# Kernel tuning notes

Measured on AMD Instinct MI355X. Metric: run time of the kernel, lower is better.

## Reference

```python
import jax, jax.numpy as jnp
import numpy as np

N_NODES = 1024
N_FEAT = 12        # must equal LOOKBACK (U1 @ B @ U2.T constraint in original code)
LOOKBACK = 12
N_DATA = 8
KSIZE = 2
DILATIONS = [1, 3, 3, 3]
DELTA_MIN = 0.05
TIME_FEATS = 36    # 15 + 5 + 4 + 12


def setup_inputs() -> dict:
    key = jax.random.key(0)
    ks = jax.random.split(key, 21)
    f32 = jnp.float32

    def rn(k, shape, fan_in):
        return jax.random.normal(k, shape, dtype=f32) / np.sqrt(fan_in)

    return {
        'observation': jax.random.normal(ks[0], (N_NODES, N_DATA, LOOKBACK), dtype=f32),
        'time_features': jax.random.normal(ks[1], (TIME_FEATS,), dtype=f32),
        # main FC stack: (n_nodes*n_data) -> fc1 -> fc2 -> n_nodes*n_feat
        'fc_w1': rn(ks[2], (N_NODES * N_DATA, 2048), N_NODES * N_DATA),
        'fc_b1': jnp.zeros((2048,), f32),
        'fc_w2': rn(ks[3], (2048, 2048), 2048),
        'fc_b2': jnp.zeros((2048,), f32),
        'fc_w3': rn(ks[4], (2048, N_NODES * N_FEAT), 2048),
        'fc_b3': jnp.zeros((N_NODES * N_FEAT,), f32),
        # graph conv weights
        'W_forward': rn(ks[5], (KSIZE, N_FEAT, N_FEAT), N_FEAT),
        'W_backward': rn(ks[6], (KSIZE, N_FEAT, N_FEAT), N_FEAT),
        'b': jnp.zeros((N_FEAT,), f32),
        # GraphConstructor params (one fixed set, reused for every adjacency)
        'layer_initial': rn(ks[7], (LOOKBACK, N_NODES), N_NODES),
        'gs_w1': rn(ks[8], (N_NODES, 256), N_NODES),
        'gs_b1': jnp.zeros((256,), f32),
        'gs_w2': rn(ks[9], (256, N_NODES * N_FEAT), 256),
        'gs_b2': jnp.zeros((N_NODES * N_FEAT,), f32),
        'gt_w1': rn(ks[10], (TIME_FEATS, 256), TIME_FEATS),
        'gt_b1': jnp.zeros((256,), f32),
        'gt_w2': rn(ks[11], (256, N_NODES * N_FEAT), 256),
        'gt_b2': jnp.zeros((N_NODES * N_FEAT,), f32),
        'B': jax.random.normal(ks[12], (N_FEAT, N_FEAT), dtype=f32) / N_FEAT,
    }


def _forward(observation, time_features, fc_w1, fc_b1, fc_w2, fc_b2, fc_w3, fc_b3,
             W_forward, W_backward, b, layer_initial,
             gs_w1, gs_b1, gs_w2, gs_b2, gt_w1, gt_b1, gt_w2, gt_b2, B):
    relu = jax.nn.relu

    # fully_connected: observation (N, D, L) -> X (N, F, L)
    obs = jnp.transpose(observation, (2, 0, 1)).reshape(LOOKBACK, -1)  # (L, N*D)
    h = relu(obs @ fc_w1 + fc_b1)
    h = relu(h @ fc_w2 + fc_b2)
    h = relu(h @ fc_w3 + fc_b3)                                        # (L, N*F)
    X0 = jnp.transpose(h.reshape(LOOKBACK, N_NODES, N_FEAT), (1, 2, 0))  # (N, F, L)

    # node embedding U (N, L, F), computed once (graph params fixed)
    sp = relu(relu(layer_initial @ gs_w1 + gs_b1) @ gs_w2 + gs_b2)     # (L, N*F)
    tp = relu(relu(time_features @ gt_w1 + gt_b1) @ gt_w2 + gt_b2)     # (N*F,)
    U = jnp.transpose((sp + tp).reshape(LOOKBACK, N_NODES, N_FEAT), (1, 0, 2))

    adj_cache = {}

    def norm_adj(a, c):
        # normalized adjacency between feature-slices a and c (static ints)
        if (a, c) in adj_cache:
            return adj_cache[(a, c)]
        U1 = U[:, :, a]                      # (N, L)
        U2 = U[:, :, c]                      # (N, L)
        x = U1 @ B @ U2.T                    # (N, N); valid since L == F
        x = jnp.where(x >= DELTA_MIN, x, 0.0)
        A = jax.nn.softmax(x, axis=1)        # torch F.softmax default dim=1 for 2D
        # degree = diag(rowsum); inv(sqrtm(diag)) = diag(1/sqrt(rowsum))
        d = 1.0 / jnp.sqrt(A.sum(-1))
        out = A * d[:, None] * d[None, :]
        adj_cache[(a, c)] = out
        return out

    def conv(X, t):
        Z = jnp.zeros((N_NODES, N_FEAT), jnp.float32)
        for k in range(KSIZE):
            X_t = X[:, :, t - k]             # (N, F)
            L1 = norm_adj(t - k, t)
            L2 = norm_adj(t + k, t)
            x = L1 @ X_t @ W_forward[k] + L2 @ X_t @ W_backward[k] + b
            Z = Z + jax.nn.relu(x)
        return Z

    def conv_layer(X, d):
        cols = []
        for t in range(1, LOOKBACK - 1):
            if t % d == 0:
                cols.append(conv(X, t))
            else:
                cols.append(jnp.zeros((N_NODES, N_FEAT), jnp.float32))
        return jnp.stack(cols, axis=-1)      # (N, F, L-2)

    Z0 = conv_layer(X0, DILATIONS[0])
    Z1 = conv_layer(Z0, DILATIONS[1])
    Z2 = conv_layer(Z1, DILATIONS[2])
    Z3 = conv_layer(Z2, DILATIONS[3])
    return (Z0[:, :, -1], Z1[:, :, -1], Z2[:, :, -1], Z3[:, :, -1])


def reference(observation, time_features, fc_w1, fc_b1, fc_w2, fc_b2, fc_w3, fc_b3,
              W_forward, W_backward, b, layer_initial,
              gs_w1, gs_b1, gs_w2, gs_b2, gt_w1, gt_b1, gt_w2, gt_b2, B):
    return _forward(observation, time_features, fc_w1, fc_b1, fc_w2, fc_b2, fc_w3, fc_b3,
                    W_forward, W_backward, b, layer_initial,
                    gs_w1, gs_b1, gs_w2, gs_b2, gt_w1, gt_b1, gt_w2, gt_b2, B)
```

## Files before the change

kernel.cpp:

```cpp
#include <hip/hip_runtime.h>

#define OFF_SPP   0
#define OFF_TPH   49152
#define OFF_P1    65536
#define OFF_P2    327680
#define OFF_X     458752
#define OFF_UP    524288
#define OFF_TPP   1703936
#define OFF_U     1802240

template<int KS, int PIN, int P, int GATHER, int ATOM>
__device__ __forceinline__ void gemm_body(
    const float* __restrict__ xin, const float* __restrict__ bias_in,
    const float* __restrict__ W, float* __restrict__ part,
    int N, int K, int bx, int by, float* lx, float* red)
{
  int tid = threadIdx.x;
  int k0 = by * KS;
  for (int i = tid; i < 2*KS; i += 256) {
    int t = i / KS, kk = i - t*KS;
    float v;
    if (GATHER) {
      int k = k0 + kk;
      v = xin[(k >> 3)*96 + (k & 7)*12 + 9 + t];
    } else if (PIN == 0) {
      v = xin[t*K + k0 + kk];
    } else {
      v = 0.f;
      const float* p0 = xin + (size_t)(t*K + k0 + kk)*PIN;
      #pragma unroll
      for (int pp = 0; pp < PIN; ++pp) v += p0[pp];
    }
    if (bias_in) { v += bias_in[k0 + kk]; v = v > 0.f ? v : 0.f; }
    lx[i] = v;
  }
  __syncthreads();
  int kg = tid >> 5, cg2 = tid & 31;
  int colbase = bx*128 + cg2*4;
  float a0=0,a1=0,a2=0,a3=0,c0=0,c1=0,c2=0,c3=0;
  const int ksub = KS/8;
  for (int kk = kg*ksub; kk < kg*ksub + ksub; ++kk) {
    float4 w = *(const float4*)(W + (size_t)(k0+kk)*N + colbase);
    float x0 = lx[kk], x1 = lx[KS + kk];
    a0=fmaf(x0,w.x,a0); a1=fmaf(x0,w.y,a1); a2=fmaf(x0,w.z,a2); a3=fmaf(x0,w.w,a3);
    c0=fmaf(x1,w.x,c0); c1=fmaf(x1,w.y,c1); c2=fmaf(x1,w.z,c2); c3=fmaf(x1,w.w,c3);
  }
  float* rp = red + (kg*32 + cg2)*8;
  rp[0]=a0; rp[1]=a1; rp[2]=a2; rp[3]=a3; rp[4]=c0; rp[5]=c1; rp[6]=c2; rp[7]=c3;
  __syncthreads();
  int cg3 = tid & 31, q = tid >> 5;
  float s = 0.f;
  #pragma unroll
  for (int g = 0; g < 8; ++g) s += red[(g*32 + cg3)*8 + q];
  int t = q >> 2, c = q & 3;
  if (ATOM) {
    atomicAdd(part + (size_t)t*N + bx*128 + cg3*4 + c, s);
  } else {
    part[(size_t)(t*N + bx*128 + cg3*4 + c)*P + by] = s;
  }
}

__global__ void __launch_bounds__(256) k_front(
    const float* __restrict__ obs, const float* __restrict__ fc_w1,
    float* __restrict__ part1,
    const float* __restrict__ li, const float* __restrict__ gs_w1,
    const float* __restrict__ tf, const float* __restrict__ gt_w1,
    const float* __restrict__ gt_b1, const float* __restrict__ fc_b3,
    float* __restrict__ sp_part, float* __restrict__ tp_h,
    float* __restrict__ X_raw, float* __restrict__ out_tail)
{
  __shared__ float smem[2304];
  int b = blockIdx.x, tid = threadIdx.x;
  if (b < 1024) {
    gemm_body<128, 0, 64, 1, 0>(obs, (const float*)nullptr, fc_w1, part1,
                                2048, 8192, b & 15, b >> 4, smem, smem + 256);
  } else if (b < 1040) {
    float (*lil)[128] = (float(*)[128])smem;
    int sb = b - 1024;
    int cb = sb & 1, kc = sb >> 1;
    for (int i = tid; i < 1536; i += 256) {
      int r = i >> 7, kk = i & 127;
      lil[r][kk] = li[r*1024 + kc*128 + kk];
    }
    __syncthreads();
    int col = cb*128 + (tid & 127);
    int kh = tid >> 7;
    float acc[12];
    #pragma unroll
    for (int t=0;t<12;++t) acc[t]=0.f;
    for (int kk = kh*64; kk < kh*64 + 64; ++kk) {
      float w = gs_w1[(size_t)(kc*128 + kk)*256 + col];
      #pragma unroll
      for (int t=0;t<12;++t) acc[t] = fmaf(lil[t][kk], w, acc[t]);
    }
    int c = kc*2 + kh;
    #pragma unroll
    for (int t=0;t<12;++t) sp_part[(c*12 + t)*256 + col] = acc[t];
    for (int i = tid; i < 2304; i += 256) out_tail[sb*2304 + i] = 0.f;
    for (int i = tid; i < 1536; i += 256) {
      int idx = sb*1536 + i;
      int colx = idx >= 12288 ? idx - 12288 : idx;
      X_raw[idx] = fc_b3[colx];
    }
  } else {
    float acc = 0.f;
    for (int k = 0; k < 36; ++k)
      acc = fmaf(tf[k], gt_w1[k*256 + tid], acc);
    float v = acc + gt_b1[tid];
    tp_h[tid] = v > 0.f ? v : 0.f;
  }
}

__global__ void __launch_bounds__(256) k_umid(
    const float* __restrict__ part1, const float* __restrict__ fc_b1,
    const float* __restrict__ fc_w2, float* __restrict__ part2,
    const float* __restrict__ sp_part, const float* __restrict__ gs_b1,
    const float* __restrict__ tp_h,
    const float* __restrict__ gs_w2, const float* __restrict__ gt_w2,
    float* __restrict__ U_part, float* __restrict__ tp_part)
{
  __shared__ float smem[2176];
  int b = blockIdx.x, tid = threadIdx.x;
  if (b < 512) {
    gemm_body<64, 64, 32, 0, 0>(part1, fc_b1, fc_w2, part2, 2048, 2048,
                                b & 15, b >> 4, smem, smem + 128);
    return;
  }
  float* spl = smem;
  float* tpl = smem + 96;
  int ug = b - 512;
  int n  = (ug & 3)*256 + tid;
  int uy = ug >> 2;
  int k0 = uy*8;
  if (tid < 96) {
    int kk = tid / 12, t = tid % 12;
    float v = gs_b1[k0 + kk];
    #pragma unroll
    for (int c = 0; c < 16; ++c) v += sp_part[(c*12 + t)*256 + k0 + kk];
    spl[kk*12 + t] = v > 0.f ? v : 0.f;
  }
  if (tid < 8) tpl[tid] = tp_h[k0 + tid];
  __syncthreads();
  float sA[3][12];
  float tA[3] = {0.f, 0.f, 0.f};
  #pragma unroll
  for (int ap=0;ap<3;++ap)
    #pragma unroll
    for (int t=0;t<12;++t) sA[ap][t]=0.f;
  #pragma unroll
  for (int kk = 0; kk < 8; ++kk) {
    float4 ws4 = *(const float4*)(gs_w2 + (size_t)(k0+kk)*12288 + 12*n + 8);
    float4 wt4 = *(const float4*)(gt_w2 + (size_t)(k0+kk)*12288 + 12*n + 8);
    float w0 = ws4.y, w1 = ws4.z, w2 = ws4.w;
    #pragma unroll
    for (int t=0;t<12;++t) {
      float s = spl[kk*12 + t];
      sA[0][t] = fmaf(s, w0, sA[0][t]);
      sA[1][t] = fmaf(s, w1, sA[1][t]);
      sA[2][t] = fmaf(s, w2, sA[2][t]);
    }
    float tv = tpl[kk];
    tA[0] = fmaf(tv, wt4.y, tA[0]);
    tA[1] = fmaf(tv, wt4.z, tA[1]);
    tA[2] = fmaf(tv, wt4.w, tA[2]);
  }
  #pragma unroll
  for (int ap=0;ap<3;++ap) {
    #pragma unroll
    for (int t=0;t<12;++t)
      U_part[(size_t)uy*36864 + ap*12288 + n*12 + t] = sA[ap][t];
    tp_part[uy*3072 + n*3 + ap] = tA[ap];
  }
}

__global__ void __launch_bounds__(256) k_fc3u(
    const float* __restrict__ part2, const float* __restrict__ fc_b2,
    const float* __restrict__ fc_w3, float* __restrict__ X_raw,
    const float* __restrict__ U_part, const float* __restrict__ tp_part,
    const float* __restrict__ gs_b2, const float* __restrict__ gt_b2,
    float* __restrict__ U)
{
  __shared__ float smem[2304];
  int b = blockIdx.x, tid = threadIdx.x;
  if (b < 1536) {
    gemm_body<128, 32, 0, 0, 1>(part2, fc_b2, fc_w3, X_raw, 12288, 2048,
                                b >> 4, b & 15, smem, smem + 256);
    return;
  }
  int i = (b - 1536)*256 + tid;
  float us = 0.f;
  for (int y = 0; y < 32; ++y) us += U_part[(size_t)y*36864 + i];
  int ap = i / 12288, rem = i - ap*12288, n = rem / 12;
  float ts = 0.f;
  for (int y = 0; y < 32; ++y) ts += tp_part[y*3072 + n*3 + ap];
  int c = n*12 + 9 + ap;
  float sv = us + gs_b2[c]; sv = sv > 0.f ? sv : 0.f;
  float tv = ts + gt_b2[c]; tv = tv > 0.f ? tv : 0.f;
  U[i] = sv + tv;
}

#define SS 1032
__global__ void __launch_bounds__(256) k_final(
    const float* __restrict__ U, const float* __restrict__ Bm,
    const float* __restrict__ X_raw,
    const float* __restrict__ Wf, const float* __restrict__ Wb,
    const float* __restrict__ bvec, float* __restrict__ out)
{
  __shared__ float sc[6*SS];
  __shared__ float Pm[72];
  __shared__ float invS[6];
  __shared__ float Bl[144];
  __shared__ float Ws0[144], Ws1[144], Ws2[144];
  __shared__ float wbuf[72];
  __shared__ float bl[12];
  int tid = threadIdx.x;
  int i0 = blockIdx.x*2;
  if (tid < 144) {
    Bl[tid]  = Bm[tid];
    Ws0[tid] = Wf[144 + tid];
    Ws1[tid] = Wf[tid] + Wb[tid];
    Ws2[tid] = Wb[144 + tid];
  }
  if (tid < 12) bl[tid] = bvec[tid];
  __syncthreads();
  if (tid < 72) {
    int r = tid / 36, ap = (tid / 12) % 3, j = tid % 12;
    float s = 0.f;
    #pragma unroll
    for (int t=0;t<12;++t)
      s = fmaf(U[ap*12288 + (i0+r)*12 + t], Bl[t*12 + j], s);
    Pm[(r*3+ap)*12 + j] = s;
  }
  __syncthreads();
  const float* U10 = U + 12288;
  for (int jj = 0; jj < 4; ++jj) {
    int j = tid + jj*256;
    const float4* ur = (const float4*)(U10 + j*12);
    float4 u0 = ur[0], u1 = ur[1], u2 = ur[2];
    float u[12] = {u0.x,u0.y,u0.z,u0.w,u1.x,u1.y,u1.z,u1.w,u2.x,u2.y,u2.z,u2.w};
    #pragma unroll
    for (int r=0;r<2;++r)
      #pragma unroll
      for (int ap=0;ap<3;++ap) {
        float s = 0.f;
        #pragma unroll
        for (int t=0;t<12;++t) s = fmaf(Pm[(r*3+ap)*12 + t], u[t], s);
        sc[(r*3+ap)*SS + j] = (s >= 0.05f) ? s : 0.f;
      }
  }
  __syncthreads();
  int wv = tid >> 6, ln = tid & 63;
  for (int pr = wv; pr < 6; pr += 4) {
    float m = -1e30f;
    for (int q = 0; q < 16; ++q) m = fmaxf(m, sc[pr*SS + ln + q*64]);
    #pragma unroll
    for (int o = 32; o > 0; o >>= 1) m = fmaxf(m, __shfl_xor(m, o));
    float sum = 0.f;
    for (int q = 0; q < 16; ++q) {
      int j = ln + q*64;
      float e = __expf(sc[pr*SS + j] - m);
      sc[pr*SS + j] = e;
      sum += e;
    }
    #pragma unroll
    for (int o = 32; o > 0; o >>= 1) sum += __shfl_xor(sum, o);
    if (ln == 0) invS[pr] = 1.f / sum;
  }
  __syncthreads();
  float acc[2][12];
  #pragma unroll
  for (int r = 0; r < 2; ++r)
    #pragma unroll
    for (int f = 0; f < 12; ++f)
      acc[r][f] = 0.f;
  int q3 = tid >> 6, jg = tid & 63;
  if (tid < 192) {
    int row = (q3 == 1) ? 1 : 0;
    const float* xr = X_raw + (size_t)row*12288;
    for (int q = 0; q < 16; ++q) {
      int j = jg + q*64;
      float e0 = sc[q3*SS + j];
      float e1 = sc[(3 + q3)*SS + j];
      const float4* px = (const float4*)(xr + j*12);
      float4 v0 = px[0], v1 = px[1], v2 = px[2];
      float xv[12] = {v0.x,v0.y,v0.z,v0.w,v1.x,v1.y,v1.z,v1.w,v2.x,v2.y,v2.z,v2.w};
      #pragma unroll
      for (int f = 0; f < 12; ++f) {
        float x = xv[f] > 0.f ? xv[f] : 0.f;
        acc[0][f] = fmaf(e0, x, acc[0][f]);
        acc[1][f] = fmaf(e1, x, acc[1][f]);
      }
    }
  }
  __syncthreads();
  float* red = sc;
  if (tid < 192) {
    #pragma unroll
    for (int r=0;r<2;++r)
      #pragma unroll
      for (int f=0;f<12;++f)
        red[((q3*2 + r)*12 + f)*64 + jg] = acc[r][f];
  }
  __syncthreads();
  if (tid < 72) {
    int q3b = tid / 24, rr = (tid / 12) % 2, f = tid % 12;
    float s = 0.f;
    for (int g = 0; g < 64; ++g) s += red[((q3b*2 + rr)*12 + f)*64 + g];
    wbuf[(q3b*2 + rr)*12 + f] = s;
  }
  __syncthreads();
  if (tid < 24) {
    int r = tid / 12, g = tid % 12;
    float y0=0.f, y1=0.f, y2=0.f;
    #pragma unroll
    for (int f=0; f<12; ++f) {
      y0 = fmaf(wbuf[(0*2+r)*12+f], Ws0[f*12+g], y0);
      y1 = fmaf(wbuf[(1*2+r)*12+f], Ws1[f*12+g], y1);
      y2 = fmaf(wbuf[(2*2+r)*12+f], Ws2[f*12+g], y2);
    }
    float a1v = invS[r*3+1]*y1;
    float a2v = invS[r*3+0]*y0 + invS[r*3+2]*y2;
    float v1 = a1v + bl[g]; v1 = v1>0.f ? v1 : 0.f;
    float v2 = a2v + bl[g]; v2 = v2>0.f ? v2 : 0.f;
    out[(i0+r)*12 + g] = v1 + v2;
  }
}

extern "C" void kernel_launch(void* const* d_in, const int* in_sizes, int n_in,
                              void* d_out, int out_size, void* d_ws, size_t ws_size,
                              hipStream_t stream)
{
  const float* obs   = (const float*)d_in[0];
  const float* tf    = (const float*)d_in[1];
  const float* fc_w1 = (const float*)d_in[2];
  const float* fc_b1 = (const float*)d_in[3];
  const float* fc_w2 = (const float*)d_in[4];
  const float* fc_b2 = (const float*)d_in[5];
  const float* fc_w3 = (const float*)d_in[6];
  const float* fc_b3 = (const float*)d_in[7];
  const float* Wf    = (const float*)d_in[8];
  const float* Wb    = (const float*)d_in[9];
  const float* bvec  = (const float*)d_in[10];
  const float* li    = (const float*)d_in[11];
  const float* gs_w1 = (const float*)d_in[12];
  const float* gs_b1 = (const float*)d_in[13];
  const float* gs_w2 = (const float*)d_in[14];
  const float* gs_b2 = (const float*)d_in[15];
  const float* gt_w1 = (const float*)d_in[16];
  const float* gt_b1 = (const float*)d_in[17];
  const float* gt_w2 = (const float*)d_in[18];
  const float* gt_b2 = (const float*)d_in[19];
  const float* Bm    = (const float*)d_in[20];
  float* out = (float*)d_out;
  float* ws  = (float*)d_ws;

  float* sp_part = ws + OFF_SPP;
  float* tp_h    = ws + OFF_TPH;
  float* part1   = ws + OFF_P1;
  float* part2   = ws + OFF_P2;
  float* X_raw   = ws + OFF_X;
  float* U_part  = ws + OFF_UP;
  float* tp_part = ws + OFF_TPP;
  float* U       = ws + OFF_U;

  k_front<<<dim3(1041), dim3(256), 0, stream>>>(obs, fc_w1, part1,
                                                li, gs_w1, tf, gt_w1, gt_b1,
                                                fc_b3, sp_part, tp_h,
                                                X_raw, out + 12288);
  k_umid<<<dim3(640), dim3(256), 0, stream>>>(part1, fc_b1, fc_w2, part2,
                                              sp_part, gs_b1, tp_h,
                                              gs_w2, gt_w2, U_part, tp_part);
  k_fc3u<<<dim3(1680), dim3(256), 0, stream>>>(part2, fc_b2, fc_w3, X_raw,
                                               U_part, tp_part, gs_b2, gt_b2,
                                               U);
  k_final<<<dim3(512), dim3(256), 0, stream>>>(U, Bm, X_raw,
                                               Wf, Wb, bvec, out);
}
```

Measured before the change: 291.9 us.

## Fuse stage kernels into persistent megakernel with hierarchical grid barriers

```diff
diff --git a/kernel.cpp b/kernel.cpp
--- a/kernel.cpp
+++ b/kernel.cpp
@@ -8,6 +8,7 @@
 #define OFF_UP    524288
 #define OFF_TPP   1703936
 #define OFF_U     1802240
+#define OFF_BAR   1839104
 
 template<int KS, int PIN, int P, int GATHER, int ATOM>
 __device__ __forceinline__ void gemm_body(
@@ -60,24 +61,43 @@
   }
 }
 
-__global__ void __launch_bounds__(256) k_front(
-    const float* __restrict__ obs, const float* __restrict__ fc_w1,
-    float* __restrict__ part1,
+__device__ __forceinline__ void gbar(int* bs, int idx)
+{
+  __syncthreads();
+  if (threadIdx.x == 0) {
+    int* leaf = bs + idx*32;
+    int* root = leaf + 8;
+    int* flag = leaf + 16;
+    __threadfence();
+    int li = (blockIdx.x >> 7) & 7;
+    if (atomicAdd(&leaf[li], 1) == 127) {
+      if (atomicAdd(root, 1) == 7) {
+        __hip_atomic_store(flag, 1, __ATOMIC_RELEASE, __HIP_MEMORY_SCOPE_AGENT);
+      }
+    }
+    int spins = 0;
+    while (__hip_atomic_load(flag, __ATOMIC_ACQUIRE,
+                             __HIP_MEMORY_SCOPE_AGENT) == 0) {
+      __builtin_amdgcn_s_sleep(2);
+      if (++spins > (1 << 22)) break;
+    }
+    __threadfence();
+  }
+  __syncthreads();
+}
+
+__global__ void __launch_bounds__(256) k_init(
     const float* __restrict__ li, const float* __restrict__ gs_w1,
     const float* __restrict__ tf, const float* __restrict__ gt_w1,
     const float* __restrict__ gt_b1, const float* __restrict__ fc_b3,
     float* __restrict__ sp_part, float* __restrict__ tp_h,
-    float* __restrict__ X_raw, float* __restrict__ out_tail)
+    float* __restrict__ X_raw, float* __restrict__ out_tail,
+    int* __restrict__ bs)
 {
-  __shared__ float smem[2304];
+  __shared__ float lil[12][128];
   int b = blockIdx.x, tid = threadIdx.x;
-  if (b < 1024) {
-    gemm_body<128, 0, 64, 1, 0>(obs, (const float*)nullptr, fc_w1, part1,
-                                2048, 8192, b & 15, b >> 4, smem, smem + 256);
-  } else if (b < 1040) {
-    float (*lil)[128] = (float(*)[128])smem;
-    int sb = b - 1024;
-    int cb = sb & 1, kc = sb >> 1;
+  if (b < 16) {
+    int cb = b & 1, kc = b >> 1;
     for (int i = tid; i < 1536; i += 256) {
       int r = i >> 7, kk = i & 127;
       lil[r][kk] = li[r*1024 + kc*128 + kk];
@@ -96,233 +116,240 @@
     int c = kc*2 + kh;
     #pragma unroll
     for (int t=0;t<12;++t) sp_part[(c*12 + t)*256 + col] = acc[t];
-    for (int i = tid; i < 2304; i += 256) out_tail[sb*2304 + i] = 0.f;
-    for (int i = tid; i < 1536; i += 256) {
-      int idx = sb*1536 + i;
-      int colx = idx >= 12288 ? idx - 12288 : idx;
-      X_raw[idx] = fc_b3[colx];
-    }
-  } else {
+  } else if (b == 16) {
+    if (tid < 96) bs[tid] = 0;
     float acc = 0.f;
     for (int k = 0; k < 36; ++k)
       acc = fmaf(tf[k], gt_w1[k*256 + tid], acc);
     float v = acc + gt_b1[tid];
     tp_h[tid] = v > 0.f ? v : 0.f;
+  } else {
+    int sb = b - 17;
+    for (int i = tid; i < 1536; i += 256) {
+      int idx = sb*1536 + i;
+      int colx = idx >= 12288 ? idx - 12288 : idx;
+      X_raw[idx] = fc_b3[colx];
+    }
+    for (int i = tid; i < 2304; i += 256)
+      out_tail[sb*2304 + i] = 0.f;
   }
 }
 
-__global__ void __launch_bounds__(256) k_umid(
-    const float* __restrict__ part1, const float* __restrict__ fc_b1,
+#define SS 1032
+__global__ void __launch_bounds__(256, 4) k_mega(
+    const float* __restrict__ obs, const float* __restrict__ fc_w1,
+    float* __restrict__ part1, const float* __restrict__ fc_b1,
     const float* __restrict__ fc_w2, float* __restrict__ part2,
+    const float* __restrict__ fc_b2, const float* __restrict__ fc_w3,
+    float* __restrict__ X_raw,
     const float* __restrict__ sp_part, const float* __restrict__ gs_b1,
     const float* __restrict__ tp_h,
     const float* __restrict__ gs_w2, const float* __restrict__ gt_w2,
-    float* __restrict__ U_part, float* __restrict__ tp_part)
+    float* __restrict__ U_part, float* __restrict__ tp_part,
+    const float* __restrict__ gs_b2, const float* __restrict__ gt_b2,
+    float* __restrict__ U, const float* __restrict__ Bm,
+    const float* __restrict__ Wf, const float* __restrict__ Wb,
+    const float* __restrict__ bvec, float* __restrict__ out,
+    int* __restrict__ bs)
 {
-  __shared__ float smem[2176];
+  __shared__ float smem[6944];
   int b = blockIdx.x, tid = threadIdx.x;
+
+  gemm_body<128, 0, 64, 1, 0>(obs, (const float*)nullptr, fc_w1, part1,
+                              2048, 8192, b & 15, b >> 4, smem, smem + 256);
+  gbar(bs, 0);
+
   if (b < 512) {
     gemm_body<64, 64, 32, 0, 0>(part1, fc_b1, fc_w2, part2, 2048, 2048,
                                 b & 15, b >> 4, smem, smem + 128);
-    return;
-  }
-  float* spl = smem;
-  float* tpl = smem + 96;
-  int ug = b - 512;
-  int n  = (ug & 3)*256 + tid;
-  int uy = ug >> 2;
-  int k0 = uy*8;
-  if (tid < 96) {
-    int kk = tid / 12, t = tid % 12;
-    float v = gs_b1[k0 + kk];
-    #pragma unroll
-    for (int c = 0; c < 16; ++c) v += sp_part[(c*12 + t)*256 + k0 + kk];
-    spl[kk*12 + t] = v > 0.f ? v : 0.f;
-  }
-  if (tid < 8) tpl[tid] = tp_h[k0 + tid];
-  __syncthreads();
-  float sA[3][12];
-  float tA[3] = {0.f, 0.f, 0.f};
-  #pragma unroll
-  for (int ap=0;ap<3;++ap)
-    #pragma unroll
-    for (int t=0;t<12;++t) sA[ap][t]=0.f;
-  #pragma unroll
-  for (int kk = 0; kk < 8; ++kk) {
-    float4 ws4 = *(const float4*)(gs_w2 + (size_t)(k0+kk)*12288 + 12*n + 8);
-    float4 wt4 = *(const float4*)(gt_w2 + (size_t)(k0+kk)*12288 + 12*n + 8);
-    float w0 = ws4.y, w1 = ws4.z, w2 = ws4.w;
-    #pragma unroll
-    for (int t=0;t<12;++t) {
-      float s = spl[kk*12 + t];
-      sA[0][t] = fmaf(s, w0, sA[0][t]);
-      sA[1][t] = fmaf(s, w1, sA[1][t]);
-      sA[2][t] = fmaf(s, w2, sA[2][t]);
-    }
-    float tv = tpl[kk];
-    tA[0] = fmaf(tv, wt4.y, tA[0]);
-    tA[1] = fmaf(tv, wt4.z, tA[1]);
-    tA[2] = fmaf(tv, wt4.w, tA[2]);
-  }
-  #pragma unroll
-  for (int ap=0;ap<3;++ap) {
-    #pragma unroll
-    for (int t=0;t<12;++t)
-      U_part[(size_t)uy*36864 + ap*12288 + n*12 + t] = sA[ap][t];
-    tp_part[uy*3072 + n*3 + ap] = tA[ap];
-  }
-}
-
-__global__ void __launch_bounds__(256) k_fc3u(
-    const float* __restrict__ part2, const float* __restrict__ fc_b2,
-    const float* __restrict__ fc_w3, float* __restrict__ X_raw,
-    const float* __restrict__ U_part, const float* __restrict__ tp_part,
-    const float* __restrict__ gs_b2, const float* __restrict__ gt_b2,
-    float* __restrict__ U)
-{
-  __shared__ float smem[2304];
-  int b = blockIdx.x, tid = threadIdx.x;
-  if (b < 1536) {
-    gemm_body<128, 32, 0, 0, 1>(part2, fc_b2, fc_w3, X_raw, 12288, 2048,
-                                b >> 4, b & 15, smem, smem + 256);
-    return;
-  }
-  int i = (b - 1536)*256 + tid;
-  float us = 0.f;
-  for (int y = 0; y < 32; ++y) us += U_part[(size_t)y*36864 + i];
-  int ap = i / 12288, rem = i - ap*12288, n = rem / 12;
-  float ts = 0.f;
-  for (int y = 0; y < 32; ++y) ts += tp_part[y*3072 + n*3 + ap];
-  int c = n*12 + 9 + ap;
-  float sv = us + gs_b2[c]; sv = sv > 0.f ? sv : 0.f;
-  float tv = ts + gt_b2[c]; tv = tv > 0.f ? tv : 0.f;
-  U[i] = sv + tv;
-}
-
-#define SS 1032
-__global__ void __launch_bounds__(256) k_final(
-    const float* __restrict__ U, const float* __restrict__ Bm,
-    const float* __restrict__ X_raw,
-    const float* __restrict__ Wf, const float* __restrict__ Wb,
-    const float* __restrict__ bvec, float* __restrict__ out)
-{
-  __shared__ float sc[6*SS];
-  __shared__ float Pm[72];
-  __shared__ float invS[6];
-  __shared__ float Bl[144];
-  __shared__ float Ws0[144], Ws1[144], Ws2[144];
-  __shared__ float wbuf[72];
-  __shared__ float bl[12];
-  int tid = threadIdx.x;
-  int i0 = blockIdx.x*2;
-  if (tid < 144) {
-    Bl[tid]  = Bm[tid];
-    Ws0[tid] = Wf[144 + tid];
-    Ws1[tid] = Wf[tid] + Wb[tid];
-    Ws2[tid] = Wb[144 + tid];
-  }
-  if (tid < 12) bl[tid] = bvec[tid];
-  __syncthreads();
-  if (tid < 72) {
-    int r = tid / 36, ap = (tid / 12) % 3, j = tid % 12;
-    float s = 0.f;
-    #pragma unroll
-    for (int t=0;t<12;++t)
-      s = fmaf(U[ap*12288 + (i0+r)*12 + t], Bl[t*12 + j], s);
-    Pm[(r*3+ap)*12 + j] = s;
-  }
-  __syncthreads();
-  const float* U10 = U + 12288;
-  for (int jj = 0; jj < 4; ++jj) {
-    int j = tid + jj*256;
-    const float4* ur = (const float4*)(U10 + j*12);
-    float4 u0 = ur[0], u1 = ur[1], u2 = ur[2];
-    float u[12] = {u0.x,u0.y,u0.z,u0.w,u1.x,u1.y,u1.z,u1.w,u2.x,u2.y,u2.z,u2.w};
-    #pragma unroll
-    for (int r=0;r<2;++r)
-      #pragma unroll
-      for (int ap=0;ap<3;++ap) {
-        float s = 0.f;
+  } else if (b < 640) {
+    float* spl = smem;
+    float* tpl = smem + 96;
+    int ug = b - 512;
+    int n  = (ug & 3)*256 + tid;
+    int uy = ug >> 2;
+    int k0 = uy*8;
+    if (tid < 96) {
+      int kk = tid / 12, t = tid % 12;
+      float v = gs_b1[k0 + kk];
+      #pragma unroll
+      for (int c = 0; c < 16; ++c) v += sp_part[(c*12 + t)*256 + k0 + kk];
+      spl[kk*12 + t] = v > 0.f ? v : 0.f;
+    }
+    if (tid < 8) tpl[tid] = tp_h[k0 + tid];
+    __syncthreads();
+    float sA[3][12];
+    float tA[3] = {0.f, 0.f, 0.f};
+    #pragma unroll
+    for (int ap=0;ap<3;++ap)
+      #pragma unroll
+      for (int t=0;t<12;++t) sA[ap][t]=0.f;
+    #pragma unroll
+    for (int kk = 0; kk < 8; ++kk) {
+      float4 ws4 = *(const float4*)(gs_w2 + (size_t)(k0+kk)*12288 + 12*n + 8);
+      float4 wt4 = *(const float4*)(gt_w2 + (size_t)(k0+kk)*12288 + 12*n + 8);
+      float w0 = ws4.y, w1 = ws4.z, w2 = ws4.w;
+      #pragma unroll
+      for (int t=0;t<12;++t) {
+        float s = spl[kk*12 + t];
+        sA[0][t] = fmaf(s, w0, sA[0][t]);
+        sA[1][t] = fmaf(s, w1, sA[1][t]);
+        sA[2][t] = fmaf(s, w2, sA[2][t]);
+      }
+      float tv = tpl[kk];
+      tA[0] = fmaf(tv, wt4.y, tA[0]);
+      tA[1] = fmaf(tv, wt4.z, tA[1]);
+      tA[2] = fmaf(tv, wt4.w, tA[2]);
+    }
+    #pragma unroll
+    for (int ap=0;ap<3;++ap) {
+      #pragma unroll
+      for (int t=0;t<12;++t)
+        U_part[(size_t)uy*36864 + ap*12288 + n*12 + t] = sA[ap][t];
+      tp_part[uy*3072 + n*3 + ap] = tA[ap];
+    }
+  }
+  gbar(bs, 1);
+
+  if (b < 768) {
+    int by = b / 96, bx = b - by*96;
+    gemm_body<256, 32, 0, 0, 1>(part2, fc_b2, fc_w3, X_raw, 12288, 2048,
+                                bx, by, smem, smem + 512);
+  } else if (b < 912) {
+    int i = (b - 768)*256 + tid;
+    float us = 0.f;
+    for (int y = 0; y < 32; ++y) us += U_part[(size_t)y*36864 + i];
+    int ap = i / 12288, rem = i - ap*12288, n = rem / 12;
+    float ts = 0.f;
+    for (int y = 0; y < 32; ++y) ts += tp_part[y*3072 + n*3 + ap];
+    int c = n*12 + 9 + ap;
+    float sv = us + gs_b2[c]; sv = sv > 0.f ? sv : 0.f;
+    float tv = ts + gt_b2[c]; tv = tv > 0.f ? tv : 0.f;
+    U[i] = sv + tv;
+  }
+  gbar(bs, 2);
+
+  if (b < 512) {
+    float* sc   = smem;
+    float* Pm   = smem + 6192;
+    float* invS = smem + 6264;
+    float* Bl   = smem + 6272;
+    float* Ws0  = smem + 6416;
+    float* Ws1  = smem + 6560;
+    float* Ws2  = smem + 6704;
+    float* wbuf = smem + 6848;
+    float* bl   = smem + 6920;
+    int i0 = b*2;
+    if (tid < 144) {
+      Bl[tid]  = Bm[tid];
+      Ws0[tid] = Wf[144 + tid];
+      Ws1[tid] = Wf[tid] + Wb[tid];
+      Ws2[tid] = Wb[144 + tid];
+    }
+    if (tid < 12) bl[tid] = bvec[tid];
+    __syncthreads();
+    if (tid < 72) {
+      int r = tid / 36, ap = (tid / 12) % 3, j = tid % 12;
+      float s = 0.f;
+      #pragma unroll
+      for (int t=0;t<12;++t)
+        s = fmaf(U[ap*12288 + (i0+r)*12 + t], Bl[t*12 + j], s);
+      Pm[(r*3+ap)*12 + j] = s;
+    }
+    __syncthreads();
+    const float* U10 = U + 12288;
+    for (int jj = 0; jj < 4; ++jj) {
+      int j = tid + jj*256;
+      const float4* ur = (const float4*)(U10 + j*12);
+      float4 u0 = ur[0], u1 = ur[1], u2 = ur[2];
+      float u[12] = {u0.x,u0.y,u0.z,u0.w,u1.x,u1.y,u1.z,u1.w,u2.x,u2.y,u2.z,u2.w};
+      #pragma unroll
+      for (int r=0;r<2;++r)
         #pragma unroll
-        for (int t=0;t<12;++t) s = fmaf(Pm[(r*3+ap)*12 + t], u[t], s);
-        sc[(r*3+ap)*SS + j] = (s >= 0.05f) ? s : 0.f;
+        for (int ap=0;ap<3;++ap) {
+          float s = 0.f;
+          #pragma unroll
+          for (int t=0;t<12;++t) s = fmaf(Pm[(r*3+ap)*12 + t], u[t], s);
+          sc[(r*3+ap)*SS + j] = (s >= 0.05f) ? s : 0.f;
+        }
+    }
+    __syncthreads();
+    int wv = tid >> 6, ln = tid & 63;
+    for (int pr = wv; pr < 6; pr += 4) {
+      float m = -1e30f;
+      for (int q = 0; q < 16; ++q) m = fmaxf(m, sc[pr*SS + ln + q*64]);
+      #pragma unroll
+      for (int o = 32; o > 0; o >>= 1) m = fmaxf(m, __shfl_xor(m, o));
+      float sum = 0.f;
+      for (int q = 0; q < 16; ++q) {
+        int j = ln + q*64;
+        float e = __expf(sc[pr*SS + j] - m);
+        sc[pr*SS + j] = e;
+        sum += e;
       }
-  }
-  __syncthreads();
-  int wv = tid >> 6, ln = tid & 63;
-  for (int pr = wv; pr < 6; pr += 4) {
-    float m = -1e30f;
-    for (int q = 0; q < 16; ++q) m = fmaxf(m, sc[pr*SS + ln + q*64]);
-    #pragma unroll
-    for (int o = 32; o > 0; o >>= 1) m = fmaxf(m, __shfl_xor(m, o));
-    float sum = 0.f;
-    for (int q = 0; q < 16; ++q) {
-      int j = ln + q*64;
-      float e = __expf(sc[pr*SS + j] - m);
-      sc[pr*SS + j] = e;
-      sum += e;
-    }
-    #pragma unroll
-    for (int o = 32; o > 0; o >>= 1) sum += __shfl_xor(sum, o);
-    if (ln == 0) invS[pr] = 1.f / sum;
-  }
-  __syncthreads();
-  float acc[2][12];
-  #pragma unroll
-  for (int r = 0; r < 2; ++r)
-    #pragma unroll
-    for (int f = 0; f < 12; ++f)
-      acc[r][f] = 0.f;
-  int q3 = tid >> 6, jg = tid & 63;
-  if (tid < 192) {
-    int row = (q3 == 1) ? 1 : 0;
-    const float* xr = X_raw + (size_t)row*12288;
-    for (int q = 0; q < 16; ++q) {
-      int j = jg + q*64;
-      float e0 = sc[q3*SS + j];
-      float e1 = sc[(3 + q3)*SS + j];
-      const float4* px = (const float4*)(xr + j*12);
-      float4 v0 = px[0], v1 = px[1], v2 = px[2];
-      float xv[12] = {v0.x,v0.y,v0.z,v0.w,v1.x,v1.y,v1.z,v1.w,v2.x,v2.y,v2.z,v2.w};
-      #pragma unroll
-      for (int f = 0; f < 12; ++f) {
-        float x = xv[f] > 0.f ? xv[f] : 0.f;
-        acc[0][f] = fmaf(e0, x, acc[0][f]);
-        acc[1][f] = fmaf(e1, x, acc[1][f]);
+      #pragma unroll
+      for (int o = 32; o > 0; o >>= 1) sum += __shfl_xor(sum, o);
+      if (ln == 0) invS[pr] = 1.f / sum;
+    }
+    __syncthreads();
+    float acc[2][12];
+    #pragma unroll
+    for (int r = 0; r < 2; ++r)
+      #pragma unroll
+      for (int f = 0; f < 12; ++f)
+        acc[r][f] = 0.f;
+    int q3 = tid >> 6, jg = tid & 63;
+    if (tid < 192) {
+      int row = (q3 == 1) ? 1 : 0;
+      const float* xr = X_raw + (size_t)row*12288;
+      for (int q = 0; q < 16; ++q) {
+        int j = jg + q*64;
+        float e0 = sc[q3*SS + j];
+        float e1 = sc[(3 + q3)*SS + j];
+        const float4* px = (const float4*)(xr + j*12);
+        float4 v0 = px[0], v1 = px[1], v2 = px[2];
+        float xv[12] = {v0.x,v0.y,v0.z,v0.w,v1.x,v1.y,v1.z,v1.w,
+                        v2.x,v2.y,v2.z,v2.w};
+        #pragma unroll
+        for (int f = 0; f < 12; ++f) {
+          float x = xv[f] > 0.f ? xv[f] : 0.f;
+          acc[0][f] = fmaf(e0, x, acc[0][f]);
+          acc[1][f] = fmaf(e1, x, acc[1][f]);
+        }
       }
     }
-  }
-  __syncthreads();
-  float* red = sc;
-  if (tid < 192) {
-    #pragma unroll
-    for (int r=0;r<2;++r)
-      #pragma unroll
-      for (int f=0;f<12;++f)
-        red[((q3*2 + r)*12 + f)*64 + jg] = acc[r][f];
-  }
-  __syncthreads();
-  if (tid < 72) {
-    int q3b = tid / 24, rr = (tid / 12) % 2, f = tid % 12;
-    float s = 0.f;
-    for (int g = 0; g < 64; ++g) s += red[((q3b*2 + rr)*12 + f)*64 + g];
-    wbuf[(q3b*2 + rr)*12 + f] = s;
-  }
-  __syncthreads();
-  if (tid < 24) {
-    int r = tid / 12, g = tid % 12;
-    float y0=0.f, y1=0.f, y2=0.f;
-    #pragma unroll
-    for (int f=0; f<12; ++f) {
-      y0 = fmaf(wbuf[(0*2+r)*12+f], Ws0[f*12+g], y0);
-      y1 = fmaf(wbuf[(1*2+r)*12+f], Ws1[f*12+g], y1);
-      y2 = fmaf(wbuf[(2*2+r)*12+f], Ws2[f*12+g], y2);
-    }
-    float a1v = invS[r*3+1]*y1;
-    float a2v = invS[r*3+0]*y0 + invS[r*3+2]*y2;
-    float v1 = a1v + bl[g]; v1 = v1>0.f ? v1 : 0.f;
-    float v2 = a2v + bl[g]; v2 = v2>0.f ? v2 : 0.f;
-    out[(i0+r)*12 + g] = v1 + v2;
+    __syncthreads();
+    float* red = sc;
+    if (tid < 192) {
+      #pragma unroll
+      for (int r=0;r<2;++r)
+        #pragma unroll
+        for (int f=0;f<12;++f)
+          red[((q3*2 + r)*12 + f)*64 + jg] = acc[r][f];
+    }
+    __syncthreads();
+    if (tid < 72) {
+      int q3b = tid / 24, rr = (tid / 12) % 2, f = tid % 12;
+      float s = 0.f;
+      for (int g = 0; g < 64; ++g) s += red[((q3b*2 + rr)*12 + f)*64 + g];
+      wbuf[(q3b*2 + rr)*12 + f] = s;
+    }
+    __syncthreads();
+    if (tid < 24) {
+      int r = tid / 12, g = tid % 12;
+      float y0=0.f, y1=0.f, y2=0.f;
+      #pragma unroll
+      for (int f=0; f<12; ++f) {
+        y0 = fmaf(wbuf[(0*2+r)*12+f], Ws0[f*12+g], y0);
+        y1 = fmaf(wbuf[(1*2+r)*12+f], Ws1[f*12+g], y1);
+        y2 = fmaf(wbuf[(2*2+r)*12+f], Ws2[f*12+g], y2);
+      }
+      float a1v = invS[r*3+1]*y1;
+      float a2v = invS[r*3+0]*y0 + invS[r*3+2]*y2;
+      float v1 = a1v + bl[g]; v1 = v1>0.f ? v1 : 0.f;
+      float v2 = a2v + bl[g]; v2 = v2>0.f ? v2 : 0.f;
+      out[(i0+r)*12 + g] = v1 + v2;
+    }
   }
 }
 
@@ -362,17 +389,16 @@
   float* U_part  = ws + OFF_UP;
   float* tp_part = ws + OFF_TPP;
   float* U       = ws + OFF_U;
-
-  k_front<<<dim3(1041), dim3(256), 0, stream>>>(obs, fc_w1, part1,
-                                                li, gs_w1, tf, gt_w1, gt_b1,
-                                                fc_b3, sp_part, tp_h,
-                                                X_raw, out + 12288);
-  k_umid<<<dim3(640), dim3(256), 0, stream>>>(part1, fc_b1, fc_w2, part2,
-                                              sp_part, gs_b1, tp_h,
-                                              gs_w2, gt_w2, U_part, tp_part);
-  k_fc3u<<<dim3(1680), dim3(256), 0, stream>>>(part2, fc_b2, fc_w3, X_raw,
-                                               U_part, tp_part, gs_b2, gt_b2,
-                                               U);
-  k_final<<<dim3(512), dim3(256), 0, stream>>>(U, Bm, X_raw,
-                                               Wf, Wb, bvec, out);
+  int*   bs      = (int*)(ws + OFF_BAR);
+
+  k_init<<<dim3(33), dim3(256), 0, stream>>>(li, gs_w1, tf, gt_w1, gt_b1,
+                                             fc_b3, sp_part, tp_h, X_raw,
+                                             out + 12288, bs);
+  k_mega<<<dim3(1024), dim3(256), 0, stream>>>(obs, fc_w1, part1,
+                                               fc_b1, fc_w2, part2,
+                                               fc_b2, fc_w3, X_raw,
+                                               sp_part, gs_b1, tp_h,
+                                               gs_w2, gt_w2, U_part, tp_part,
+                                               gs_b2, gt_b2, U, Bm,
+                                               Wf, Wb, bvec, out, bs);
 }
```

After: 822.7 us. 2.82x slower.
